# Kernel tuning notes

Measured on AMD Instinct MI355X. Metric: run time of the kernel, lower is better.

## Reference

```python
import jax, jax.numpy as jnp
import numpy as np

INPUT_DIM = 256
HIDDEN_DIM = 1024
OUTPUT_DIM = 256
B, T = 128, 1024


def setup_inputs() -> dict:
    key = jax.random.key(0)
    ks = jax.random.split(key, 7)
    std = 1.0 / np.sqrt(HIDDEN_DIM)
    u = lambda k, shape: jax.random.uniform(k, shape, jnp.float32, -std, std)
    return {
        "x": jax.random.normal(ks[0], (B, T, INPUT_DIM), jnp.float32),
        "Wx": u(ks[1], (2 * HIDDEN_DIM, INPUT_DIM)),   # x2h weight
        "bx": u(ks[2], (2 * HIDDEN_DIM,)),             # x2h bias
        "Wh": u(ks[3], (HIDDEN_DIM, HIDDEN_DIM)),      # h2h weight
        "bh": u(ks[4], (HIDDEN_DIM,)),                 # h2h bias
        "Wfc": u(ks[5], (OUTPUT_DIM, HIDDEN_DIM)),     # fc weight
        "bfc": u(ks[6], (OUTPUT_DIM,)),                # fc bias
    }


def _run(x, Wx, bx, Wh, bh, Wfc, bfc):
    bsz = x.shape[0]
    h0 = jnp.zeros((bsz, HIDDEN_DIM), x.dtype)
    # Precompute input gates for all timesteps in one big GEMM: [B,T,2H]
    gate_x_all = jnp.einsum("bti,gi->btg", x, Wx) + bx

    def step(h, gate_x):
        gate_h = h @ Wh.T + bh                       # [B,H]
        i_r, i_i = jnp.split(gate_x, 2, axis=-1)     # each [B,H]
        resetgate = jax.nn.sigmoid(i_r)
        inputgate = jax.nn.sigmoid(i_i)
        newgate = jnp.tanh(resetgate * gate_h)
        hy = newgate + inputgate * (h - newgate)
        return hy, None

    # scan over time: gate_x_all transposed to [T,B,2H]
    h_last, _ = jax.lax.scan(step, h0, jnp.swapaxes(gate_x_all, 0, 1))
    return h_last @ Wfc.T + bfc                      # [B, OUTPUT_DIM]


def reference(x, Wx, bx, Wh, bh, Wfc, bfc):
    return _run(x, Wx, bx, Wh, bh, Wfc, bfc)
```

## Files before the change

### kernel.cpp

```cpp
#include <hip/hip_runtime.h>
#include <hip/hip_fp16.h>


#define BB 128
#define TT 1024
#define ID 256
#define HH 1024

using f16   = _Float16;
using f16x8 = __attribute__((ext_vector_type(8))) _Float16;
using f32x4 = __attribute__((ext_vector_type(4))) float;
typedef unsigned long long u64;

#define OFF_X    0
#define OFF_GX   16384
#define OFF_GH   25088
#define LDS_SIZE 42496

#define SWZ(row, kbyte) ((kbyte) ^ (((row) & 3) << 4))
#define MFMA16(a, b, c) __builtin_amdgcn_mfma_f32_16x16x32_f16(a, b, c, 0, 0, 0)

static __device__ __forceinline__ void store4h(f16* dst, float a, float b, float c, float d) {
  union { f16 h[4]; u64 u; } p;
  p.h[0] = (f16)a; p.h[1] = (f16)b; p.h[2] = (f16)c; p.h[3] = (f16)d;
  *reinterpret_cast<u64*>(dst) = p.u;
}

static __device__ __forceinline__ f16x8 cvt8(float4 a, float4 b) {
  f16x8 r;
  r[0] = (f16)a.x; r[1] = (f16)a.y; r[2] = (f16)a.z; r[3] = (f16)a.w;
  r[4] = (f16)b.x; r[5] = (f16)b.y; r[6] = (f16)b.z; r[7] = (f16)b.w;
  return r;
}

static __device__ __forceinline__ void put_tile(float* dst, f32x4 v, int lane) {
  const int c = lane & 15, r4 = (lane >> 4) * 4;
  #pragma unroll
  for (int r = 0; r < 4; ++r) dst[(r4 + r) * 17 + c] = v[r];
}

__global__ __launch_bounds__(256, 1) void rnn_core(
    const float* __restrict__ x, const float* __restrict__ Wx, const float* __restrict__ bx,
    const float* __restrict__ Wh, const float* __restrict__ bh,
    f16* __restrict__ hbuf,
    float* __restrict__ hfin,
    int* __restrict__ flags)
{
  extern __shared__ char lds[];
  char*  xbuf = lds + OFF_X;
  float* gxch = (float*)(lds + OFF_GX);
  float* ghT  = (float*)(lds + OFF_GH);

  const int tid  = threadIdx.x;
  const int lane = tid & 63;
  const int w    = tid >> 6;
  const int g    = blockIdx.x & 7;
  const int cw   = blockIdx.x >> 3;
  const int b0   = g * 16;
  const int j0   = cw * 32;
  const int col  = lane & 15;
  const int quad = lane >> 4;
  const int row4 = quad * 4;
  const int nt   = w >> 1;

  f16x8 whf[16];
  #pragma unroll
  for (int n = 0; n < 2; ++n)
    #pragma unroll
    for (int i = 0; i < 8; ++i) {
      const float* p = Wh + (size_t)(j0 + n * 16 + col) * HH + ((w << 3) + i) * 32 + quad * 8;
      whf[n * 8 + i] = cvt8(*reinterpret_cast<const float4*>(p),
                            *reinterpret_cast<const float4*>(p + 4));
    }
  f16x8 wxf[16];
  if (w & 1) {
    #pragma unroll
    for (int g2 = 0; g2 < 2; ++g2)
      #pragma unroll
      for (int ks = 0; ks < 8; ++ks) {
        const float* p = Wx + (size_t)(g2 * HH + j0 + nt * 16 + col) * ID + ks * 32 + quad * 8;
        wxf[g2 * 8 + ks] = cvt8(*reinterpret_cast<const float4*>(p),
                                *reinterpret_cast<const float4*>(p + 4));
      }
  }

  for (int s = 0; s < 2; ++s)
    for (int c = tid; c < 1024; c += 256) {
      int row = c >> 6, k4 = c & 63;
      float4 v = *reinterpret_cast<const float4*>(
          x + ((size_t)(b0 + row) * TT + s) * ID + k4 * 4);
      store4h((f16*)(xbuf + s * 8192 + row * 512 + SWZ(row, k4 * 8)), v.x, v.y, v.z, v.w);
    }
  __syncthreads();

  if (w & 1) {
    const char* pxb = xbuf + col * 512 + ((quad * 16) ^ ((col & 3) << 4));
    f32x4 a0 = {0,0,0,0}, a1 = {0,0,0,0};
    #pragma unroll
    for (int ks = 0; ks < 8; ++ks) {
      f16x8 bfr = *reinterpret_cast<const f16x8*>(pxb + ks * 64);
      a0 = MFMA16(wxf[ks], bfr, a0);
      a1 = MFMA16(wxf[8 + ks], bfr, a1);
    }
    put_tile(gxch + nt * 272, a0, lane);
    put_tile(gxch + (2 + nt) * 272, a1, lane);
  }

  float4 bh4 = {0,0,0,0}, bxr4 = {0,0,0,0}, bxi4 = {0,0,0,0};
  if (!(w & 1)) {
    bh4  = *reinterpret_cast<const float4*>(bh + j0 + nt * 16 + row4);
    bxr4 = *reinterpret_cast<const float4*>(bx + j0 + nt * 16 + row4);
    bxi4 = *reinterpret_cast<const float4*>(bx + HH + j0 + nt * 16 + row4);
  }
  float hm[4] = {0.f, 0.f, 0.f, 0.f};

  const unsigned gvo = (unsigned)(col * 64 + quad * 16);
  const u64 hb0 = (u64)((const char*)hbuf + (((size_t)g * 32 + (w << 3)) << 10)) + gvo;
  const u64 hb1 = hb0 + (256ull << 10);
  const u64 pb0 = (u64)((char*)hbuf + (((size_t)g * 32 + cw) << 10))
                  + (unsigned)(col * 64 + nt * 32 + quad * 8);
  const u64 pb1 = pb0 + (256ull << 10);
  int* myflag = flags + ((g * 32 + cw) * 2 + nt) * 16;
  const int* pollp = flags + ((g * 32 + (w << 3) + (lane & 7)) * 2 + ((lane >> 3) & 1)) * 16;

  for (int t = 0; t < TT; ++t) {
    const int p = t & 1;
    f32x4 acc0 = {0,0,0,0}, acc1 = {0,0,0,0};
    if (t > 0) {
      int v;
      do { v = (lane < 16)
               ? __hip_atomic_load(pollp, __ATOMIC_RELAXED, __HIP_MEMORY_SCOPE_SYSTEM) : t;
      } while (!__all(v >= t));

      u64 ad0 = p ? hb1 : hb0;
      u64 ad1 = ad0 + 4096;
      f32x4 f0, f1, f2, f3, f4, f5, f6, f7;
      asm volatile(
        "global_load_dwordx4 %0, %8, off sc0 sc1\n\t"
        "global_load_dwordx4 %1, %8, off offset:1024 sc0 sc1\n\t"
        "global_load_dwordx4 %2, %8, off offset:2048 sc0 sc1\n\t"
        "global_load_dwordx4 %3, %8, off offset:3072 sc0 sc1\n\t"
        "global_load_dwordx4 %4, %9, off sc0 sc1\n\t"
        "global_load_dwordx4 %5, %9, off offset:1024 sc0 sc1\n\t"
        "global_load_dwordx4 %6, %9, off offset:2048 sc0 sc1\n\t"
        "global_load_dwordx4 %7, %9, off offset:3072 sc0 sc1\n\t"
        "s_waitcnt vmcnt(0)"
        : "=&v"(f0), "=&v"(f1), "=&v"(f2), "=&v"(f3),
          "=&v"(f4), "=&v"(f5), "=&v"(f6), "=&v"(f7)
        : "v"(ad0), "v"(ad1) : "memory");

      #define STEPM(i, F) { f16x8 bf_ = *reinterpret_cast<f16x8*>(&F); \
        acc0 = MFMA16(whf[i], bf_, acc0); acc1 = MFMA16(whf[8 + (i)], bf_, acc1); }
      STEPM(0, f0) STEPM(1, f1) STEPM(2, f2) STEPM(3, f3)
      STEPM(4, f4) STEPM(5, f5) STEPM(6, f6) STEPM(7, f7)
      #undef STEPM
    }
    float* ghp = ghT + p * 2176;
    if (w == 0)      { put_tile(ghp + (4 + 0) * 272, acc1, lane); }
    else if (w == 1) { put_tile(ghp + 1 * 272, acc0, lane);
                       put_tile(ghp + (4 + 1) * 272, acc1, lane); }
    else if (w == 2) { put_tile(ghp + 2 * 272, acc0, lane); }
    else             { put_tile(ghp + 3 * 272, acc0, lane);
                       put_tile(ghp + (4 + 3) * 272, acc1, lane); }

    __syncthreads();

    if (!(w & 1)) {
      const float* basep = ghp + nt * 4 * 272;
      const float* s0 = basep + ((w == 0) ? 1 : 0) * 272;
      const float* s1 = basep + ((w == 0) ? 2 : 1) * 272;
      const float* s2 = basep + 3 * 272;
      const float* gxr = gxch + p * 1088 + nt * 272;
      const float* gxi = gxch + p * 1088 + (2 + nt) * 272;
      f32x4 own = (w == 0) ? acc0 : acc1;
      float hn[4];
      #pragma unroll
      for (int r = 0; r < 4; ++r) {
        int idx = (row4 + r) * 17 + col;
        float ghf = own[r] + s0[idx] + s1[idx] + s2[idx] + ((const float*)&bh4)[r];
        float ir  = gxr[idx] + ((const float*)&bxr4)[r];
        float ii  = gxi[idx] + ((const float*)&bxi4)[r];
        float rg  = 1.f / (1.f + __expf(-ir));
        float ig  = 1.f / (1.f + __expf(-ii));
        float z   = rg * ghf;
        z = fminf(fmaxf(z, -15.f), 15.f);
        float e   = __expf(-2.f * z);
        float ng  = (1.f - e) / (1.f + e);
        float h_  = ng + ig * (hm[r] - ng);
        hm[r] = h_; hn[r] = h_;
      }
      union { f16 h[4]; u64 uu; } pk;
      pk.h[0] = (f16)hn[0]; pk.h[1] = (f16)hn[1]; pk.h[2] = (f16)hn[2]; pk.h[3] = (f16)hn[3];
      u64* adp = (u64*)(p ? pb0 : pb1);
      __hip_atomic_store(adp, pk.uu, __ATOMIC_RELAXED, __HIP_MEMORY_SCOPE_SYSTEM);
      asm volatile("s_waitcnt vmcnt(0)" ::: "memory");
      if (lane == 0)
        __hip_atomic_store(myflag, t + 1, __ATOMIC_RELAXED, __HIP_MEMORY_SCOPE_SYSTEM);
    } else {
      if (t + 1 < TT) {
        const char* pxb = xbuf + ((t + 1) & 1) * 8192 + col * 512
                          + ((quad * 16) ^ ((col & 3) << 4));
        f32x4 a0 = {0,0,0,0}, a1 = {0,0,0,0};
        #pragma unroll
        for (int ks = 0; ks < 8; ++ks) {
          f16x8 bfr = *reinterpret_cast<const f16x8*>(pxb + ks * 64);
          a0 = MFMA16(wxf[ks], bfr, a0);
          a1 = MFMA16(wxf[8 + ks], bfr, a1);
        }
        float* gdst = gxch + ((t + 1) & 1) * 1088;
        put_tile(gdst + nt * 272, a0, lane);
        put_tile(gdst + (2 + nt) * 272, a1, lane);
      }
      if (t + 2 < TT) {
        char* xd = xbuf + p * 8192;
        #pragma unroll
        for (int it = 0; it < 8; ++it) {
          int row = nt * 8 + it;
          float4 v = *reinterpret_cast<const float4*>(
              x + ((size_t)(b0 + row) * TT + (t + 2)) * ID + lane * 4);
          store4h((f16*)(xd + row * 512 + SWZ(row, lane * 8)), v.x, v.y, v.z, v.w);
        }
      }
    }
  }

  if (!(w & 1)) {
    float4 o; o.x = hm[0]; o.y = hm[1]; o.z = hm[2]; o.w = hm[3];
    *reinterpret_cast<float4*>(hfin + (size_t)(b0 + col) * HH + j0 + nt * 16 + row4) = o;
  }
}

__global__ __launch_bounds__(64) void fc_kernel(
    const float* __restrict__ hfin, const float* __restrict__ Wfc,
    const float* __restrict__ bfc, float* __restrict__ out)
{
  const int lane = threadIdx.x;
  const int mb = blockIdx.x >> 4, nb = blockIdx.x & 15;
  const int col = lane & 15, row4 = (lane >> 4) * 4;
  const float* pa = hfin + (size_t)(mb * 16 + (lane & 15)) * HH + (lane >> 4) * 8;
  const float* pb = Wfc  + (size_t)(nb * 16 + (lane & 15)) * HH + (lane >> 4) * 8;
  f32x4 acc = {0.f, 0.f, 0.f, 0.f};
  for (int kc = 0; kc < 32; ++kc) {
    f16x8 a, b;
    #pragma unroll
    for (int e = 0; e < 8; ++e) {
      a[e] = (f16)pa[kc * 32 + e];
      b[e] = (f16)pb[kc * 32 + e];
    }
    acc = __builtin_amdgcn_mfma_f32_16x16x32_f16(a, b, acc, 0, 0, 0);
  }
  float bias = bfc[nb * 16 + col];
  #pragma unroll
  for (int r = 0; r < 4; ++r)
    out[(size_t)(mb * 16 + row4 + r) * 256 + nb * 16 + col] = acc[r] + bias;
}

extern "C" void kernel_launch(void* const* d_in, const int* in_sizes, int n_in,
                              void* d_out, int out_size, void* d_ws, size_t ws_size,
                              hipStream_t stream) {
  const float* x   = (const float*)d_in[0];
  const float* Wx  = (const float*)d_in[1];
  const float* bx  = (const float*)d_in[2];
  const float* Wh  = (const float*)d_in[3];
  const float* bh  = (const float*)d_in[4];
  const float* Wfc = (const float*)d_in[5];
  const float* bfc = (const float*)d_in[6];
  float* out = (float*)d_out;

  char* ws = (char*)d_ws;
  f16*   hbuf  = (f16*)ws;
  float* hfin  = (float*)(ws + 524288);
  int*   flags = (int*)(ws + 1048576);

  hipMemsetAsync(flags, 0, 32768, stream);

  (void)hipFuncSetAttribute((const void*)rnn_core,
                            hipFuncAttributeMaxDynamicSharedMemorySize, LDS_SIZE);

  void* args[8];
  args[0] = (void*)&x;    args[1] = (void*)&Wx;   args[2] = (void*)&bx;
  args[3] = (void*)&Wh;   args[4] = (void*)&bh;   args[5] = (void*)&hbuf;
  args[6] = (void*)&hfin; args[7] = (void*)&flags;
  hipError_t err = hipLaunchCooperativeKernel((void*)rnn_core, dim3(256), dim3(256),
                                              args, LDS_SIZE, stream);
  if (err != hipSuccess) {
    rnn_core<<<dim3(256), dim3(256), LDS_SIZE, stream>>>(x, Wx, bx, Wh, bh, hbuf, hfin, flags);
  }

  fc_kernel<<<dim3(128), dim3(64), 0, stream>>>(hfin, Wfc, bfc, out);
}
```

Before: 3.083 ms.

## Halve persistent blocks, give every wave gate math and x-projection in registers

Each block now owns 64 hidden columns instead of 32, so the grid shrinks from 256 to 128 cooperative blocks. All four waves do the recurrent GEMM over four column tiles, perform the gate nonlinearity, and keep the input-projection results in registers rather than an LDS staging buffer. The aim is fewer blocks to synchronise through global flags each timestep and no split between compute and prefetch waves. In exchange each wave does twice the Wh MFMA work, holds 32 weight fragments in registers, polls 64 flags per group, and needs more LDS for the cross-wave reduction.

```diff
diff --git a/kernel.cpp b/kernel.cpp
--- a/kernel.cpp
+++ b/kernel.cpp
@@ -13,9 +13,8 @@
 typedef unsigned long long u64;
 
 #define OFF_X    0
-#define OFF_GX   16384
-#define OFF_GH   25088
-#define LDS_SIZE 42496
+#define OFF_GH   16384
+#define LDS_SIZE 51200
 
 #define SWZ(row, kbyte) ((kbyte) ^ (((row) & 3) << 4))
 #define MFMA16(a, b, c) __builtin_amdgcn_mfma_f32_16x16x32_f16(a, b, c, 0, 0, 0)
@@ -48,7 +47,6 @@
 {
   extern __shared__ char lds[];
   char*  xbuf = lds + OFF_X;
-  float* gxch = (float*)(lds + OFF_GX);
   float* ghT  = (float*)(lds + OFF_GH);
 
   const int tid  = threadIdx.x;
@@ -57,32 +55,33 @@
   const int g    = blockIdx.x & 7;
   const int cw   = blockIdx.x >> 3;
   const int b0   = g * 16;
-  const int j0   = cw * 32;
+  const int j0   = cw * 64;
   const int col  = lane & 15;
   const int quad = lane >> 4;
   const int row4 = quad * 4;
-  const int nt   = w >> 1;
-
-  f16x8 whf[16];
-  #pragma unroll
-  for (int n = 0; n < 2; ++n)
+
+  f16x8 whf[32];
+  #pragma unroll
+  for (int nt = 0; nt < 4; ++nt)
     #pragma unroll
     for (int i = 0; i < 8; ++i) {
-      const float* p = Wh + (size_t)(j0 + n * 16 + col) * HH + ((w << 3) + i) * 32 + quad * 8;
-      whf[n * 8 + i] = cvt8(*reinterpret_cast<const float4*>(p),
-                            *reinterpret_cast<const float4*>(p + 4));
+      const float* p = Wh + (size_t)(j0 + nt * 16 + col) * HH + ((w << 3) + i) * 32 + quad * 8;
+      whf[nt * 8 + i] = cvt8(*reinterpret_cast<const float4*>(p),
+                             *reinterpret_cast<const float4*>(p + 4));
     }
   f16x8 wxf[16];
-  if (w & 1) {
-    #pragma unroll
-    for (int g2 = 0; g2 < 2; ++g2)
-      #pragma unroll
-      for (int ks = 0; ks < 8; ++ks) {
-        const float* p = Wx + (size_t)(g2 * HH + j0 + nt * 16 + col) * ID + ks * 32 + quad * 8;
-        wxf[g2 * 8 + ks] = cvt8(*reinterpret_cast<const float4*>(p),
-                                *reinterpret_cast<const float4*>(p + 4));
-      }
-  }
+  #pragma unroll
+  for (int gt = 0; gt < 2; ++gt)
+    #pragma unroll
+    for (int ks = 0; ks < 8; ++ks) {
+      const float* p = Wx + (size_t)(gt * HH + j0 + w * 16 + col) * ID + ks * 32 + quad * 8;
+      wxf[gt * 8 + ks] = cvt8(*reinterpret_cast<const float4*>(p),
+                              *reinterpret_cast<const float4*>(p + 4));
+    }
+
+  const float4 bh4  = *reinterpret_cast<const float4*>(bh + j0 + w * 16 + row4);
+  const float4 bxr4 = *reinterpret_cast<const float4*>(bx + j0 + w * 16 + row4);
+  const float4 bxi4 = *reinterpret_cast<const float4*>(bx + HH + j0 + w * 16 + row4);
 
   for (int s = 0; s < 2; ++s)
     for (int c = tid; c < 1024; c += 256) {
@@ -93,43 +92,35 @@
     }
   __syncthreads();
 
-  if (w & 1) {
+  f32x4 gxr0 = {0,0,0,0}, gxi0 = {0,0,0,0}, gxr1 = {0,0,0,0}, gxi1 = {0,0,0,0};
+  {
     const char* pxb = xbuf + col * 512 + ((quad * 16) ^ ((col & 3) << 4));
-    f32x4 a0 = {0,0,0,0}, a1 = {0,0,0,0};
     #pragma unroll
     for (int ks = 0; ks < 8; ++ks) {
       f16x8 bfr = *reinterpret_cast<const f16x8*>(pxb + ks * 64);
-      a0 = MFMA16(wxf[ks], bfr, a0);
-      a1 = MFMA16(wxf[8 + ks], bfr, a1);
-    }
-    put_tile(gxch + nt * 272, a0, lane);
-    put_tile(gxch + (2 + nt) * 272, a1, lane);
-  }
-
-  float4 bh4 = {0,0,0,0}, bxr4 = {0,0,0,0}, bxi4 = {0,0,0,0};
-  if (!(w & 1)) {
-    bh4  = *reinterpret_cast<const float4*>(bh + j0 + nt * 16 + row4);
-    bxr4 = *reinterpret_cast<const float4*>(bx + j0 + nt * 16 + row4);
-    bxi4 = *reinterpret_cast<const float4*>(bx + HH + j0 + nt * 16 + row4);
-  }
+      gxr0 = MFMA16(wxf[ks], bfr, gxr0);
+      gxi0 = MFMA16(wxf[8 + ks], bfr, gxi0);
+    }
+  }
+
   float hm[4] = {0.f, 0.f, 0.f, 0.f};
 
   const unsigned gvo = (unsigned)(col * 64 + quad * 16);
-  const u64 hb0 = (u64)((const char*)hbuf + (((size_t)g * 32 + (w << 3)) << 10)) + gvo;
-  const u64 hb1 = hb0 + (256ull << 10);
-  const u64 pb0 = (u64)((char*)hbuf + (((size_t)g * 32 + cw) << 10))
-                  + (unsigned)(col * 64 + nt * 32 + quad * 8);
-  const u64 pb1 = pb0 + (256ull << 10);
-  int* myflag = flags + ((g * 32 + cw) * 2 + nt) * 16;
-  const int* pollp = flags + ((g * 32 + (w << 3) + (lane & 7)) * 2 + ((lane >> 3) & 1)) * 16;
+  const u64 hb0 = (u64)((const char*)hbuf + (size_t)g * 32768 + (size_t)w * 8192) + gvo;
+  const u64 hb1 = hb0 + 262144;
+  const int kp  = ((w & 1) << 4) + row4;
+  const u64 pb0 = (u64)((char*)hbuf + (size_t)g * 32768 + (size_t)cw * 2048
+                        + (w >> 1) * 1024 + col * 64 + (kp >> 3) * 16 + (kp & 7) * 2);
+  const u64 pb1 = pb0 + 262144;
+  int* myflag = flags + ((g * 64) + cw * 4 + w) * 16;
+  const int* pollp = flags + ((g * 64) + lane) * 16;
 
   for (int t = 0; t < TT; ++t) {
     const int p = t & 1;
-    f32x4 acc0 = {0,0,0,0}, acc1 = {0,0,0,0};
+    f32x4 a0 = {0,0,0,0}, a1 = {0,0,0,0}, a2 = {0,0,0,0}, a3 = {0,0,0,0};
     if (t > 0) {
       int v;
-      do { v = (lane < 16)
-               ? __hip_atomic_load(pollp, __ATOMIC_RELAXED, __HIP_MEMORY_SCOPE_SYSTEM) : t;
+      do { v = __hip_atomic_load(pollp, __ATOMIC_RELAXED, __HIP_MEMORY_SCOPE_SYSTEM);
       } while (!__all(v >= t));
 
       u64 ad0 = p ? hb1 : hb0;
@@ -150,39 +141,38 @@
         : "v"(ad0), "v"(ad1) : "memory");
 
       #define STEPM(i, F) { f16x8 bf_ = *reinterpret_cast<f16x8*>(&F); \
-        acc0 = MFMA16(whf[i], bf_, acc0); acc1 = MFMA16(whf[8 + (i)], bf_, acc1); }
+        a0 = MFMA16(whf[i], bf_, a0);      a1 = MFMA16(whf[8 + (i)], bf_, a1); \
+        a2 = MFMA16(whf[16 + (i)], bf_, a2); a3 = MFMA16(whf[24 + (i)], bf_, a3); }
       STEPM(0, f0) STEPM(1, f1) STEPM(2, f2) STEPM(3, f3)
       STEPM(4, f4) STEPM(5, f5) STEPM(6, f6) STEPM(7, f7)
       #undef STEPM
     }
-    float* ghp = ghT + p * 2176;
-    if (w == 0)      { put_tile(ghp + (4 + 0) * 272, acc1, lane); }
-    else if (w == 1) { put_tile(ghp + 1 * 272, acc0, lane);
-                       put_tile(ghp + (4 + 1) * 272, acc1, lane); }
-    else if (w == 2) { put_tile(ghp + 2 * 272, acc0, lane); }
-    else             { put_tile(ghp + 3 * 272, acc0, lane);
-                       put_tile(ghp + (4 + 3) * 272, acc1, lane); }
+    float* ghp = ghT + p * 4352;
+    if (w != 0) put_tile(ghp + (w * 4 + 0) * 272, a0, lane);
+    if (w != 1) put_tile(ghp + (w * 4 + 1) * 272, a1, lane);
+    if (w != 2) put_tile(ghp + (w * 4 + 2) * 272, a2, lane);
+    if (w != 3) put_tile(ghp + (w * 4 + 3) * 272, a3, lane);
 
     __syncthreads();
 
-    if (!(w & 1)) {
-      const float* basep = ghp + nt * 4 * 272;
-      const float* s0 = basep + ((w == 0) ? 1 : 0) * 272;
-      const float* s1 = basep + ((w == 0) ? 2 : 1) * 272;
-      const float* s2 = basep + 3 * 272;
-      const float* gxr = gxch + p * 1088 + nt * 272;
-      const float* gxi = gxch + p * 1088 + (2 + nt) * 272;
-      f32x4 own = (w == 0) ? acc0 : acc1;
+    {
+      f32x4 own = (w == 0) ? a0 : ((w == 1) ? a1 : ((w == 2) ? a2 : a3));
+      f32x4 cgr = p ? gxr1 : gxr0;
+      f32x4 cgi = p ? gxi1 : gxi0;
       float hn[4];
       #pragma unroll
       for (int r = 0; r < 4; ++r) {
         int idx = (row4 + r) * 17 + col;
-        float ghf = own[r] + s0[idx] + s1[idx] + s2[idx] + ((const float*)&bh4)[r];
-        float ir  = gxr[idx] + ((const float*)&bxr4)[r];
-        float ii  = gxi[idx] + ((const float*)&bxi4)[r];
+        float s = own[r] + ((const float*)&bh4)[r];
+        if (w != 0) s += ghp[(0 * 4 + w) * 272 + idx];
+        if (w != 1) s += ghp[(1 * 4 + w) * 272 + idx];
+        if (w != 2) s += ghp[(2 * 4 + w) * 272 + idx];
+        if (w != 3) s += ghp[(3 * 4 + w) * 272 + idx];
+        float ir  = cgr[r] + ((const float*)&bxr4)[r];
+        float ii  = cgi[r] + ((const float*)&bxi4)[r];
         float rg  = 1.f / (1.f + __expf(-ir));
         float ig  = 1.f / (1.f + __expf(-ii));
-        float z   = rg * ghf;
+        float z   = rg * s;
         z = fminf(fmaxf(z, -15.f), 15.f);
         float e   = __expf(-2.f * z);
         float ng  = (1.f - e) / (1.f + e);
@@ -196,37 +186,34 @@
       asm volatile("s_waitcnt vmcnt(0)" ::: "memory");
       if (lane == 0)
         __hip_atomic_store(myflag, t + 1, __ATOMIC_RELAXED, __HIP_MEMORY_SCOPE_SYSTEM);
-    } else {
-      if (t + 1 < TT) {
-        const char* pxb = xbuf + ((t + 1) & 1) * 8192 + col * 512
-                          + ((quad * 16) ^ ((col & 3) << 4));
-        f32x4 a0 = {0,0,0,0}, a1 = {0,0,0,0};
-        #pragma unroll
-        for (int ks = 0; ks < 8; ++ks) {
-          f16x8 bfr = *reinterpret_cast<const f16x8*>(pxb + ks * 64);
-          a0 = MFMA16(wxf[ks], bfr, a0);
-          a1 = MFMA16(wxf[8 + ks], bfr, a1);
-        }
-        float* gdst = gxch + ((t + 1) & 1) * 1088;
-        put_tile(gdst + nt * 272, a0, lane);
-        put_tile(gdst + (2 + nt) * 272, a1, lane);
+    }
+    if (t + 1 < TT) {
+      f32x4 tr = {0,0,0,0}, ti = {0,0,0,0};
+      const char* pxb = xbuf + (p ^ 1) * 8192 + col * 512 + ((quad * 16) ^ ((col & 3) << 4));
+      #pragma unroll
+      for (int ks = 0; ks < 8; ++ks) {
+        f16x8 bfr = *reinterpret_cast<const f16x8*>(pxb + ks * 64);
+        tr = MFMA16(wxf[ks], bfr, tr);
+        ti = MFMA16(wxf[8 + ks], bfr, ti);
       }
-      if (t + 2 < TT) {
-        char* xd = xbuf + p * 8192;
-        #pragma unroll
-        for (int it = 0; it < 8; ++it) {
-          int row = nt * 8 + it;
-          float4 v = *reinterpret_cast<const float4*>(
-              x + ((size_t)(b0 + row) * TT + (t + 2)) * ID + lane * 4);
-          store4h((f16*)(xd + row * 512 + SWZ(row, lane * 8)), v.x, v.y, v.z, v.w);
-        }
+      if (p) { gxr0 = tr; gxi0 = ti; } else { gxr1 = tr; gxi1 = ti; }
+    }
+    if (t + 2 < TT) {
+      char* xd = xbuf + p * 8192;
+      #pragma unroll
+      for (int it = 0; it < 4; ++it) {
+        int c = tid + it * 256;
+        int row = c >> 6, k4 = c & 63;
+        float4 v = *reinterpret_cast<const float4*>(
+            x + ((size_t)(b0 + row) * TT + (t + 2)) * ID + k4 * 4);
+        store4h((f16*)(xd + row * 512 + SWZ(row, k4 * 8)), v.x, v.y, v.z, v.w);
       }
     }
   }
 
-  if (!(w & 1)) {
+  {
     float4 o; o.x = hm[0]; o.y = hm[1]; o.z = hm[2]; o.w = hm[3];
-    *reinterpret_cast<float4*>(hfin + (size_t)(b0 + col) * HH + j0 + nt * 16 + row4) = o;
+    *reinterpret_cast<float4*>(hfin + (size_t)(b0 + col) * HH + j0 + w * 16 + row4) = o;
   }
 }
 
@@ -281,10 +268,10 @@
   args[0] = (void*)&x;    args[1] = (void*)&Wx;   args[2] = (void*)&bx;
   args[3] = (void*)&Wh;   args[4] = (void*)&bh;   args[5] = (void*)&hbuf;
   args[6] = (void*)&hfin; args[7] = (void*)&flags;
-  hipError_t err = hipLaunchCooperativeKernel((void*)rnn_core, dim3(256), dim3(256),
+  hipError_t err = hipLaunchCooperativeKernel((void*)rnn_core, dim3(128), dim3(256),
                                               args, LDS_SIZE, stream);
   if (err != hipSuccess) {
-    rnn_core<<<dim3(256), dim3(256), LDS_SIZE, stream>>>(x, Wx, bx, Wh, bh, hbuf, hfin, flags);
+    rnn_core<<<dim3(128), dim3(256), LDS_SIZE, stream>>>(x, Wx, bx, Wh, bh, hbuf, hfin, flags);
   }
 
   fc_kernel<<<dim3(128), dim3(64), 0, stream>>>(hfin, Wfc, bfc, out);
```

Result: slower. 4.271 ms (+38.5%).

## Replace flag polling with sentinel-tagged data polling over triple-buffered hidden state

Applied to the files above, without the earlier changes.

Drops the separate per-block flag array. Consumers now poll the hidden-state data directly and retry until no 0xFFFF sentinel half remains, using three rotating buffers where the slot two steps ahead is reset to the sentinel. This removes one round trip per step (a flag load, then a data load) and the extra wait-then-flag-store on the producer side. The risk is that an f16 value whose bits are 0xFFFF (a NaN) would stall the loop, and the check only covers two of the four u64 words in each load. Correctness also depends on the ordering between the sentinel reset and the reuse of that slot.

```diff
diff --git a/kernel.cpp b/kernel.cpp
--- a/kernel.cpp
+++ b/kernel.cpp
@@ -19,6 +19,8 @@
 
 #define SWZ(row, kbyte) ((kbyte) ^ (((row) & 3) << 4))
 #define MFMA16(a, b, c) __builtin_amdgcn_mfma_f32_16x16x32_f16(a, b, c, 0, 0, 0)
+#define OKH(F) (((__float_as_uint((F).y) >> 16) != 0xFFFFu) && \
+                ((__float_as_uint((F).w) >> 16) != 0xFFFFu))
 
 static __device__ __forceinline__ void store4h(f16* dst, float a, float b, float c, float d) {
   union { f16 h[4]; u64 u; } p;
@@ -43,8 +45,7 @@
     const float* __restrict__ x, const float* __restrict__ Wx, const float* __restrict__ bx,
     const float* __restrict__ Wh, const float* __restrict__ bh,
     f16* __restrict__ hbuf,
-    float* __restrict__ hfin,
-    int* __restrict__ flags)
+    float* __restrict__ hfin)
 {
   extern __shared__ char lds[];
   char*  xbuf = lds + OFF_X;
@@ -115,46 +116,44 @@
   float hm[4] = {0.f, 0.f, 0.f, 0.f};
 
   const unsigned gvo = (unsigned)(col * 64 + quad * 16);
-  const u64 hb0 = (u64)((const char*)hbuf + (((size_t)g * 32 + (w << 3)) << 10)) + gvo;
-  const u64 hb1 = hb0 + (256ull << 10);
-  const u64 pb0 = (u64)((char*)hbuf + (((size_t)g * 32 + cw) << 10))
-                  + (unsigned)(col * 64 + nt * 32 + quad * 8);
-  const u64 pb1 = pb0 + (256ull << 10);
-  int* myflag = flags + ((g * 32 + cw) * 2 + nt) * 16;
-  const int* pollp = flags + ((g * 32 + (w << 3) + (lane & 7)) * 2 + ((lane >> 3) & 1)) * 16;
-
+  const u64 gbase = (u64)((const char*)hbuf + (((size_t)g * 32 + (w << 3)) << 10)) + gvo;
+  u64 gA = gbase, gB = gbase + 262144, gC = gbase + 524288;
+  const u64 pbase = (u64)((char*)hbuf + (((size_t)g * 32 + cw) << 10))
+                    + (unsigned)(col * 64 + nt * 32 + quad * 8);
+  u64 pA = pbase, pB = pbase + 262144, pC = pbase + 524288;
   for (int t = 0; t < TT; ++t) {
     const int p = t & 1;
     f32x4 acc0 = {0,0,0,0}, acc1 = {0,0,0,0};
     if (t > 0) {
-      int v;
-      do { v = (lane < 16)
-               ? __hip_atomic_load(pollp, __ATOMIC_RELAXED, __HIP_MEMORY_SCOPE_SYSTEM) : t;
-      } while (!__all(v >= t));
-
-      u64 ad0 = p ? hb1 : hb0;
-      u64 ad1 = ad0 + 4096;
+      u64 ad0 = gA, ad1 = gA + 4096;
       f32x4 f0, f1, f2, f3, f4, f5, f6, f7;
-      asm volatile(
-        "global_load_dwordx4 %0, %8, off sc0 sc1\n\t"
-        "global_load_dwordx4 %1, %8, off offset:1024 sc0 sc1\n\t"
-        "global_load_dwordx4 %2, %8, off offset:2048 sc0 sc1\n\t"
-        "global_load_dwordx4 %3, %8, off offset:3072 sc0 sc1\n\t"
-        "global_load_dwordx4 %4, %9, off sc0 sc1\n\t"
-        "global_load_dwordx4 %5, %9, off offset:1024 sc0 sc1\n\t"
-        "global_load_dwordx4 %6, %9, off offset:2048 sc0 sc1\n\t"
-        "global_load_dwordx4 %7, %9, off offset:3072 sc0 sc1\n\t"
-        "s_waitcnt vmcnt(0)"
-        : "=&v"(f0), "=&v"(f1), "=&v"(f2), "=&v"(f3),
-          "=&v"(f4), "=&v"(f5), "=&v"(f6), "=&v"(f7)
-        : "v"(ad0), "v"(ad1) : "memory");
-
+      for (;;) {
+        asm volatile(
+          "global_load_dwordx4 %0, %8, off sc0 sc1\n\t"
+          "global_load_dwordx4 %1, %8, off offset:1024 sc0 sc1\n\t"
+          "global_load_dwordx4 %2, %8, off offset:2048 sc0 sc1\n\t"
+          "global_load_dwordx4 %3, %8, off offset:3072 sc0 sc1\n\t"
+          "global_load_dwordx4 %4, %9, off sc0 sc1\n\t"
+          "global_load_dwordx4 %5, %9, off offset:1024 sc0 sc1\n\t"
+          "global_load_dwordx4 %6, %9, off offset:2048 sc0 sc1\n\t"
+          "global_load_dwordx4 %7, %9, off offset:3072 sc0 sc1\n\t"
+          "s_waitcnt vmcnt(0)"
+          : "=&v"(f0), "=&v"(f1), "=&v"(f2), "=&v"(f3),
+            "=&v"(f4), "=&v"(f5), "=&v"(f6), "=&v"(f7)
+          : "v"(ad0), "v"(ad1) : "memory");
+        bool ok = OKH(f0) && OKH(f1) && OKH(f2) && OKH(f3)
+               && OKH(f4) && OKH(f5) && OKH(f6) && OKH(f7);
+        if (__all(ok)) break;
+      }
       #define STEPM(i, F) { f16x8 bf_ = *reinterpret_cast<f16x8*>(&F); \
         acc0 = MFMA16(whf[i], bf_, acc0); acc1 = MFMA16(whf[8 + (i)], bf_, acc1); }
       STEPM(0, f0) STEPM(1, f1) STEPM(2, f2) STEPM(3, f3)
       STEPM(4, f4) STEPM(5, f5) STEPM(6, f6) STEPM(7, f7)
       #undef STEPM
     }
+    if (!(w & 1))
+      __hip_atomic_store((u64*)pC, ~0ull, __ATOMIC_RELAXED, __HIP_MEMORY_SCOPE_SYSTEM);
+
     float* ghp = ghT + p * 2176;
     if (w == 0)      { put_tile(ghp + (4 + 0) * 272, acc1, lane); }
     else if (w == 1) { put_tile(ghp + 1 * 272, acc0, lane);
@@ -191,11 +190,8 @@
       }
       union { f16 h[4]; u64 uu; } pk;
       pk.h[0] = (f16)hn[0]; pk.h[1] = (f16)hn[1]; pk.h[2] = (f16)hn[2]; pk.h[3] = (f16)hn[3];
-      u64* adp = (u64*)(p ? pb0 : pb1);
-      __hip_atomic_store(adp, pk.uu, __ATOMIC_RELAXED, __HIP_MEMORY_SCOPE_SYSTEM);
       asm volatile("s_waitcnt vmcnt(0)" ::: "memory");
-      if (lane == 0)
-        __hip_atomic_store(myflag, t + 1, __ATOMIC_RELAXED, __HIP_MEMORY_SCOPE_SYSTEM);
+      __hip_atomic_store((u64*)pB, pk.uu, __ATOMIC_RELAXED, __HIP_MEMORY_SCOPE_SYSTEM);
     } else {
       if (t + 1 < TT) {
         const char* pxb = xbuf + ((t + 1) & 1) * 8192 + col * 512
@@ -222,6 +218,8 @@
         }
       }
     }
+    { u64 tg = gA; gA = gB; gB = gC; gC = tg;
+      u64 tp = pA; pA = pB; pB = pC; pC = tp; }
   }
 
   if (!(w & 1)) {
@@ -268,23 +266,22 @@
   float* out = (float*)d_out;
 
   char* ws = (char*)d_ws;
-  f16*   hbuf  = (f16*)ws;
-  float* hfin  = (float*)(ws + 524288);
-  int*   flags = (int*)(ws + 1048576);
-
-  hipMemsetAsync(flags, 0, 32768, stream);
+  f16*   hbuf = (f16*)ws;
+  float* hfin = (float*)(ws + 786432);
+
+  hipMemsetAsync(hbuf, 0xFF, 786432, stream);
 
   (void)hipFuncSetAttribute((const void*)rnn_core,
                             hipFuncAttributeMaxDynamicSharedMemorySize, LDS_SIZE);
 
-  void* args[8];
+  void* args[7];
   args[0] = (void*)&x;    args[1] = (void*)&Wx;   args[2] = (void*)&bx;
   args[3] = (void*)&Wh;   args[4] = (void*)&bh;   args[5] = (void*)&hbuf;
-  args[6] = (void*)&hfin; args[7] = (void*)&flags;
+  args[6] = (void*)&hfin;
   hipError_t err = hipLaunchCooperativeKernel((void*)rnn_core, dim3(256), dim3(256),
                                               args, LDS_SIZE, stream);
   if (err != hipSuccess) {
-    rnn_core<<<dim3(256), dim3(256), LDS_SIZE, stream>>>(x, Wx, bx, Wh, bh, hbuf, hfin, flags);
+    rnn_core<<<dim3(256), dim3(256), LDS_SIZE, stream>>>(x, Wx, bx, Wh, bh, hbuf, hfin);
   }
 
   fc_kernel<<<dim3(128), dim3(64), 0, stream>>>(hfin, Wfc, bfc, out);
```

Measured after the change: 4.864 ms. +57.8%, slower.
